# Performance work log

Measured on AMD Instinct MI355X. Metric: run time of the kernel, lower is better.

The kernel has to match this reference:

```python
import jax, jax.numpy as jnp
import numpy as np

B, N, D_IN, D_MEM, LAYERS = 8, 2048, 128, 128, 3


def setup_inputs() -> dict:
    key = jax.random.key(0)
    k1, k2, k3, k4 = jax.random.split(key, 4)
    inputs = jax.random.normal(k1, (B, N, D_IN), dtype=jnp.float32)
    # attention-derived adjacency: nonnegative weights
    out_adj = jax.random.uniform(k2, (B, N, N), dtype=jnp.float32)
    # per-layer Linear weights (all layers 128->128 here, stacked) with
    # torch nn.Linear-style init scale 1/sqrt(fan_in)
    scale = 1.0 / np.sqrt(D_IN)
    W = jax.random.uniform(k3, (LAYERS, D_IN, D_MEM), minval=-scale, maxval=scale, dtype=jnp.float32)
    b = jax.random.uniform(k4, (LAYERS, D_MEM), minval=-scale, maxval=scale, dtype=jnp.float32)
    return {"inputs": inputs, "out_adj": out_adj, "W": W, "b": b}


def reference(inputs, out_adj, W, b):
    # GCN.forward (eval mode; dropout = identity)
    adj = out_adj  # [B, N, N]
    denom = jnp.sum(adj, axis=2, keepdims=True) + 1.0  # [B, N, 1]
    outputs = inputs  # [B, N, D]
    for l in range(W.shape[0]):
        Ax = jnp.einsum('bij,bjd->bid', adj, outputs)      # aggregate
        AxW = Ax @ W[l] + b[l]                             # per-layer linear
        outputs = jax.nn.relu(AxW / denom)                 # normalize + activate
    return outputs
```

## Files before the change

### kernel.cpp

```cpp
#include <hip/hip_runtime.h>

#define NN 2048
#define DD 128

typedef _Float16 f16x8 __attribute__((ext_vector_type(8)));
typedef float f32x4 __attribute__((ext_vector_type(4)));

__global__ __launch_bounds__(256) void prep_kernel(
    const float* __restrict__ W, _Float16* __restrict__ Wt) {
  int idx = blockIdx.x * 256 + threadIdx.x;
  int l = idx >> 14, r = idx & 16383, d = r >> 7, k = r & 127;
  Wt[idx] = (_Float16)W[l * 16384 + k * 128 + d];
}

__global__ __launch_bounds__(256) void gemmY_kernel(
    const float* __restrict__ X, const _Float16* __restrict__ Wt,
    _Float16* __restrict__ Yt) {
  const int bx = blockIdx.x;
  const int batch = bx & 7, n0 = (bx >> 3) * 32;
  const int tid = threadIdx.x, lane = tid & 63, wave = tid >> 6;
  const int quad = lane >> 4, l15 = lane & 15, d0 = wave * 32;
  const float* Xb = X + (size_t)(batch * NN + n0) * DD;
  f32x4 acc[2][2] = {};
#pragma unroll
  for (int kk = 0; kk < 128; kk += 32) {
    f16x8 a0 = *(const f16x8*)(Wt + (d0 + l15) * DD + kk + quad * 8);
    f16x8 a1 = *(const f16x8*)(Wt + (d0 + 16 + l15) * DD + kk + quad * 8);
#pragma unroll
    for (int fi = 0; fi < 2; ++fi) {
      const float* xp = Xb + (size_t)(fi * 16 + l15) * DD + kk + quad * 8;
      float4 x0 = *(const float4*)xp;
      float4 x1 = *(const float4*)(xp + 4);
      f16x8 b = {(_Float16)x0.x, (_Float16)x0.y, (_Float16)x0.z, (_Float16)x0.w,
                 (_Float16)x1.x, (_Float16)x1.y, (_Float16)x1.z, (_Float16)x1.w};
      acc[0][fi] = __builtin_amdgcn_mfma_f32_16x16x32_f16(a0, b, acc[0][fi], 0, 0, 0);
      acc[1][fi] = __builtin_amdgcn_mfma_f32_16x16x32_f16(a1, b, acc[1][fi], 0, 0, 0);
    }
  }
  _Float16* YtB = Yt + (size_t)batch * DD * NN;
#pragma unroll
  for (int df = 0; df < 2; ++df)
#pragma unroll
    for (int fi = 0; fi < 2; ++fi)
#pragma unroll
      for (int r = 0; r < 4; ++r)
        YtB[(size_t)(d0 + df * 16 + quad * 4 + r) * NN + n0 + fi * 16 + l15] =
            (_Float16)acc[df][fi][r];
}

template<bool LAST>
__global__ __launch_bounds__(256) void agg_kernel(
    const float* __restrict__ adj, const _Float16* __restrict__ Yt,
    const float* __restrict__ bias, const _Float16* __restrict__ Wn,
    _Float16* __restrict__ Ytn, float* __restrict__ out) {
  __shared__ _Float16 Bs[2][32 * 64];
  __shared__ float Xs[32][132];
  __shared__ float bsh[128];
  __shared__ float rd[32];

  const int tid = threadIdx.x, bx = blockIdx.x;
  const int batch = bx & 7, i0 = (bx >> 3) * 32;
  const int lane = tid & 63, wave = tid >> 6;
  const int quad = lane >> 4, l15 = lane & 15, d0 = wave * 32;
  const int ai = tid >> 3, ac = tid & 7;
  const int sc = ac ^ (ai & 7);

  const float* adjR = adj + (size_t)(batch * NN + i0 + ai) * NN + ac * 8;
  const _Float16* YtB = Yt + (size_t)batch * DD * NN;
  const _Float16* Ya0 = YtB + (size_t)(d0 + l15) * NN;
  const _Float16* Ya1 = YtB + (size_t)(d0 + 16 + l15) * NN;

  if (tid < 128) bsh[tid] = bias[tid];

  f32x4 acc[2][2] = {};
  float rowsum = 0.f;

  float4 av0 = *(const float4*)(adjR);
  float4 av1 = *(const float4*)(adjR + 4);
  f16x8 a[2][2];
#pragma unroll
  for (int k2 = 0; k2 < 2; ++k2) {
    a[k2][0] = *(const f16x8*)(Ya0 + k2 * 32 + quad * 8);
    a[k2][1] = *(const f16x8*)(Ya1 + k2 * 32 + quad * 8);
  }

  for (int ko = 0; ko < 32; ++ko) {
    rowsum += ((av0.x + av0.y) + (av0.z + av0.w)) + ((av1.x + av1.y) + (av1.z + av1.w));
    f16x8 h = {(_Float16)av0.x, (_Float16)av0.y, (_Float16)av0.z, (_Float16)av0.w,
               (_Float16)av1.x, (_Float16)av1.y, (_Float16)av1.z, (_Float16)av1.w};
    *(f16x8*)(&Bs[ko & 1][ai * 64 + sc * 8]) = h;
    f16x8 an[2][2];
    if (ko < 31) {
      const int kb = (ko + 1) * 64;
      av0 = *(const float4*)(adjR + kb);
      av1 = *(const float4*)(adjR + kb + 4);
#pragma unroll
      for (int k2 = 0; k2 < 2; ++k2) {
        an[k2][0] = *(const f16x8*)(Ya0 + kb + k2 * 32 + quad * 8);
        an[k2][1] = *(const f16x8*)(Ya1 + kb + k2 * 32 + quad * 8);
      }
    }
    __syncthreads();
    const _Float16* B = Bs[ko & 1];
#pragma unroll
    for (int k2 = 0; k2 < 2; ++k2)
#pragma unroll
      for (int fi = 0; fi < 2; ++fi) {
        const int row = fi * 16 + l15;
        const int ch = (k2 * 4 + quad) ^ (row & 7);
        f16x8 b = *(const f16x8*)(&B[row * 64 + ch * 8]);
        acc[0][fi] = __builtin_amdgcn_mfma_f32_16x16x32_f16(a[k2][0], b, acc[0][fi], 0, 0, 0);
        acc[1][fi] = __builtin_amdgcn_mfma_f32_16x16x32_f16(a[k2][1], b, acc[1][fi], 0, 0, 0);
      }
#pragma unroll
    for (int k2 = 0; k2 < 2; ++k2) { a[k2][0] = an[k2][0]; a[k2][1] = an[k2][1]; }
  }

  rowsum += __shfl_xor(rowsum, 1);
  rowsum += __shfl_xor(rowsum, 2);
  rowsum += __shfl_xor(rowsum, 4);
  if (ac == 0) rd[ai] = 1.0f / (rowsum + 1.0f);
  __syncthreads();

#pragma unroll
  for (int df = 0; df < 2; ++df)
#pragma unroll
    for (int fi = 0; fi < 2; ++fi)
#pragma unroll
      for (int r = 0; r < 4; ++r) {
        int d = d0 + df * 16 + quad * 4 + r;
        int i = fi * 16 + l15;
        Xs[i][d] = fmaxf((acc[df][fi][r] + bsh[d]) * rd[i], 0.f);
      }
  __syncthreads();

  if (LAST) {
    float* outB = out + (size_t)(batch * NN + i0) * DD;
#pragma unroll
    for (int u = 0; u < 4; ++u) {
      int c = tid + 256 * u;
      int i = c >> 5, f4 = (c & 31) * 4;
      *(float4*)(outB + (size_t)i * DD + f4) = *(const float4*)&Xs[i][f4];
    }
  } else {
    f32x4 acc2[2][2] = {};
#pragma unroll
    for (int kk = 0; kk < 128; kk += 32) {
      f16x8 a0 = *(const f16x8*)(Wn + (d0 + l15) * DD + kk + quad * 8);
      f16x8 a1 = *(const f16x8*)(Wn + (d0 + 16 + l15) * DD + kk + quad * 8);
#pragma unroll
      for (int fi = 0; fi < 2; ++fi) {
        const float* xp = &Xs[fi * 16 + l15][kk + quad * 8];
        f16x8 b = {(_Float16)xp[0], (_Float16)xp[1], (_Float16)xp[2], (_Float16)xp[3],
                   (_Float16)xp[4], (_Float16)xp[5], (_Float16)xp[6], (_Float16)xp[7]};
        acc2[0][fi] = __builtin_amdgcn_mfma_f32_16x16x32_f16(a0, b, acc2[0][fi], 0, 0, 0);
        acc2[1][fi] = __builtin_amdgcn_mfma_f32_16x16x32_f16(a1, b, acc2[1][fi], 0, 0, 0);
      }
    }
    _Float16* YnB = Ytn + (size_t)batch * DD * NN;
#pragma unroll
    for (int df = 0; df < 2; ++df)
#pragma unroll
      for (int fi = 0; fi < 2; ++fi)
#pragma unroll
        for (int r = 0; r < 4; ++r)
          YnB[(size_t)(d0 + df * 16 + quad * 4 + r) * NN + i0 + fi * 16 + l15] =
              (_Float16)acc2[df][fi][r];
  }
}

extern "C" void kernel_launch(void* const* d_in, const int* in_sizes, int n_in,
                              void* d_out, int out_size, void* d_ws, size_t ws_size,
                              hipStream_t stream) {
  const float* x0   = (const float*)d_in[0];
  const float* adj  = (const float*)d_in[1];
  const float* W    = (const float*)d_in[2];
  const float* bias = (const float*)d_in[3];
  float* out = (float*)d_out;

  _Float16* Wt   = (_Float16*)d_ws;
  _Float16* YtA  = (_Float16*)((char*)d_ws + 131072);
  _Float16* YtB_ = (_Float16*)d_out;

  dim3 blk(256);
  prep_kernel <<<192, blk, 0, stream>>>(W, Wt);
  gemmY_kernel<<<512, blk, 0, stream>>>(x0, Wt, YtA);
  agg_kernel<false><<<512, blk, 0, stream>>>(adj, YtA,  bias,       Wt + 16384, YtB_, nullptr);
  agg_kernel<false><<<512, blk, 0, stream>>>(adj, YtB_, bias + 128, Wt + 32768, YtA,  nullptr);
  agg_kernel<true ><<<512, blk, 0, stream>>>(adj, YtA,  bias + 256, nullptr,    nullptr, out);
}
```

Measured before the change: 290.0 us.

## Cache fp16 adjacency and row normalizers on first layer, reuse in later layers

The first aggregation layer writes the fp16-converted adjacency tile and the per-row reciprocal normalizers to workspace. A new fp16 aggregation kernel then reads that half-size adjacency directly into MFMA fragments, with no LDS staging or barriers, for layers two and three. This halves adjacency read traffic for those layers at the cost of an extra 64 MB write in layer one. It needs a large workspace and falls back to the old path when the workspace is too small.

```diff
diff --git a/kernel.cpp b/kernel.cpp
--- a/kernel.cpp
+++ b/kernel.cpp
@@ -48,11 +48,12 @@
             (_Float16)acc[df][fi][r];
 }
 
-template<bool LAST>
+template<bool SAVE, bool LAST>
 __global__ __launch_bounds__(256) void agg_kernel(
     const float* __restrict__ adj, const _Float16* __restrict__ Yt,
     const float* __restrict__ bias, const _Float16* __restrict__ Wn,
-    _Float16* __restrict__ Ytn, float* __restrict__ out) {
+    _Float16* __restrict__ Ytn, float* __restrict__ out,
+    _Float16* __restrict__ adjH, float* __restrict__ rdg) {
   __shared__ _Float16 Bs[2][32 * 64];
   __shared__ float Xs[32][132];
   __shared__ float bsh[128];
@@ -69,6 +70,7 @@
   const _Float16* YtB = Yt + (size_t)batch * DD * NN;
   const _Float16* Ya0 = YtB + (size_t)(d0 + l15) * NN;
   const _Float16* Ya1 = YtB + (size_t)(d0 + 16 + l15) * NN;
+  _Float16* AdjHW = SAVE ? adjH + (size_t)(batch * NN + i0 + ai) * NN + ac * 8 : nullptr;
 
   if (tid < 128) bsh[tid] = bias[tid];
 
@@ -89,6 +91,7 @@
     f16x8 h = {(_Float16)av0.x, (_Float16)av0.y, (_Float16)av0.z, (_Float16)av0.w,
                (_Float16)av1.x, (_Float16)av1.y, (_Float16)av1.z, (_Float16)av1.w};
     *(f16x8*)(&Bs[ko & 1][ai * 64 + sc * 8]) = h;
+    if (SAVE) *(f16x8*)(AdjHW + ko * 64) = h;
     f16x8 an[2][2];
     if (ko < 31) {
       const int kb = (ko + 1) * 64;
@@ -119,7 +122,11 @@
   rowsum += __shfl_xor(rowsum, 1);
   rowsum += __shfl_xor(rowsum, 2);
   rowsum += __shfl_xor(rowsum, 4);
-  if (ac == 0) rd[ai] = 1.0f / (rowsum + 1.0f);
+  if (ac == 0) {
+    float v = 1.0f / (rowsum + 1.0f);
+    rd[ai] = v;
+    if (SAVE) rdg[batch * NN + i0 + ai] = v;
+  }
   __syncthreads();
 
 #pragma unroll
@@ -131,6 +138,114 @@
         int d = d0 + df * 16 + quad * 4 + r;
         int i = fi * 16 + l15;
         Xs[i][d] = fmaxf((acc[df][fi][r] + bsh[d]) * rd[i], 0.f);
+      }
+  __syncthreads();
+
+  if (LAST) {
+    float* outB = out + (size_t)(batch * NN + i0) * DD;
+#pragma unroll
+    for (int u = 0; u < 4; ++u) {
+      int c = tid + 256 * u;
+      int i = c >> 5, f4 = (c & 31) * 4;
+      *(float4*)(outB + (size_t)i * DD + f4) = *(const float4*)&Xs[i][f4];
+    }
+  } else {
+    f32x4 acc2[2][2] = {};
+#pragma unroll
+    for (int kk = 0; kk < 128; kk += 32) {
+      f16x8 a0 = *(const f16x8*)(Wn + (d0 + l15) * DD + kk + quad * 8);
+      f16x8 a1 = *(const f16x8*)(Wn + (d0 + 16 + l15) * DD + kk + quad * 8);
+#pragma unroll
+      for (int fi = 0; fi < 2; ++fi) {
+        const float* xp = &Xs[fi * 16 + l15][kk + quad * 8];
+        f16x8 b = {(_Float16)xp[0], (_Float16)xp[1], (_Float16)xp[2], (_Float16)xp[3],
+                   (_Float16)xp[4], (_Float16)xp[5], (_Float16)xp[6], (_Float16)xp[7]};
+        acc2[0][fi] = __builtin_amdgcn_mfma_f32_16x16x32_f16(a0, b, acc2[0][fi], 0, 0, 0);
+        acc2[1][fi] = __builtin_amdgcn_mfma_f32_16x16x32_f16(a1, b, acc2[1][fi], 0, 0, 0);
+      }
+    }
+    _Float16* YnB = Ytn + (size_t)batch * DD * NN;
+#pragma unroll
+    for (int df = 0; df < 2; ++df)
+#pragma unroll
+      for (int fi = 0; fi < 2; ++fi)
+#pragma unroll
+        for (int r = 0; r < 4; ++r)
+          YnB[(size_t)(d0 + df * 16 + quad * 4 + r) * NN + i0 + fi * 16 + l15] =
+              (_Float16)acc2[df][fi][r];
+  }
+}
+
+__device__ __forceinline__ void loadf16(f16x8 (&AF)[2][2], f16x8 (&BF)[2][2],
+    const _Float16* Ya0, const _Float16* Ya1,
+    const _Float16* Ba0, const _Float16* Ba1, int kb) {
+#pragma unroll
+  for (int k2 = 0; k2 < 2; ++k2) {
+    AF[k2][0] = *(const f16x8*)(Ya0 + kb + k2 * 32);
+    AF[k2][1] = *(const f16x8*)(Ya1 + kb + k2 * 32);
+    BF[k2][0] = *(const f16x8*)(Ba0 + kb + k2 * 32);
+    BF[k2][1] = *(const f16x8*)(Ba1 + kb + k2 * 32);
+  }
+}
+
+__device__ __forceinline__ void mfma8(const f16x8 (&AF)[2][2],
+    const f16x8 (&BF)[2][2], f32x4 (&acc)[2][2]) {
+#pragma unroll
+  for (int k2 = 0; k2 < 2; ++k2)
+#pragma unroll
+    for (int fi = 0; fi < 2; ++fi) {
+      acc[0][fi] = __builtin_amdgcn_mfma_f32_16x16x32_f16(AF[k2][0], BF[k2][fi], acc[0][fi], 0, 0, 0);
+      acc[1][fi] = __builtin_amdgcn_mfma_f32_16x16x32_f16(AF[k2][1], BF[k2][fi], acc[1][fi], 0, 0, 0);
+    }
+}
+
+template<bool LAST>
+__global__ __launch_bounds__(256) void aggf16_kernel(
+    const _Float16* __restrict__ adjH, const float* __restrict__ rdg,
+    const _Float16* __restrict__ Yt, const float* __restrict__ bias,
+    const _Float16* __restrict__ Wn, _Float16* __restrict__ Ytn,
+    float* __restrict__ out) {
+  __shared__ float Xs[32][132];
+
+  const int tid = threadIdx.x, bx = blockIdx.x;
+  const int batch = bx & 7, i0 = (bx >> 3) * 32;
+  const int lane = tid & 63, wave = tid >> 6;
+  const int quad = lane >> 4, l15 = lane & 15, d0 = wave * 32;
+
+  const _Float16* YtB = Yt + (size_t)batch * DD * NN;
+  const _Float16* Ya0 = YtB + (size_t)(d0 + l15) * NN + quad * 8;
+  const _Float16* Ya1 = YtB + (size_t)(d0 + 16 + l15) * NN + quad * 8;
+  const _Float16* AdjB = adjH + (size_t)(batch * NN + i0) * NN;
+  const _Float16* Ba0 = AdjB + (size_t)l15 * NN + quad * 8;
+  const _Float16* Ba1 = AdjB + (size_t)(16 + l15) * NN + quad * 8;
+
+  const float* rdb = rdg + batch * NN + i0;
+  float rdv0 = rdb[l15], rdv1 = rdb[16 + l15];
+  float4 bv0 = *(const float4*)(bias + d0 + quad * 4);
+  float4 bv1 = *(const float4*)(bias + d0 + 16 + quad * 4);
+
+  f32x4 acc[2][2] = {};
+  f16x8 aA[2][2], bA[2][2], aB[2][2], bB[2][2];
+
+  loadf16(aA, bA, Ya0, Ya1, Ba0, Ba1, 0);
+#pragma unroll
+  for (int ko = 0; ko < 32; ko += 2) {
+    if (ko + 1 < 32) loadf16(aB, bB, Ya0, Ya1, Ba0, Ba1, (ko + 1) * 64);
+    mfma8(aA, bA, acc);
+    if (ko + 2 < 32) loadf16(aA, bA, Ya0, Ya1, Ba0, Ba1, (ko + 2) * 64);
+    mfma8(aB, bB, acc);
+  }
+
+#pragma unroll
+  for (int df = 0; df < 2; ++df)
+#pragma unroll
+    for (int fi = 0; fi < 2; ++fi)
+#pragma unroll
+      for (int r = 0; r < 4; ++r) {
+        int d = d0 + df * 16 + quad * 4 + r;
+        float bia = df ? ((const float*)&bv1)[r] : ((const float*)&bv0)[r];
+        float rv = fi ? rdv1 : rdv0;
+        Xs[fi * 16 + l15][d] = fmaxf((acc[df][fi][r] + bia) * rv, 0.f);
       }
   __syncthreads();
 
@@ -180,12 +295,22 @@
 
   _Float16* Wt   = (_Float16*)d_ws;
   _Float16* YtA  = (_Float16*)((char*)d_ws + 131072);
+  float*    rdg  = (float*)((char*)d_ws + 131072 + (4u << 20));
+  _Float16* adjH = (_Float16*)((char*)d_ws + (8u << 20));
   _Float16* YtB_ = (_Float16*)d_out;
+
+  const bool big = ws_size >= ((8ull + 64ull) << 20);
 
   dim3 blk(256);
   prep_kernel <<<192, blk, 0, stream>>>(W, Wt);
   gemmY_kernel<<<512, blk, 0, stream>>>(x0, Wt, YtA);
-  agg_kernel<false><<<512, blk, 0, stream>>>(adj, YtA,  bias,       Wt + 16384, YtB_, nullptr);
-  agg_kernel<false><<<512, blk, 0, stream>>>(adj, YtB_, bias + 128, Wt + 32768, YtA,  nullptr);
-  agg_kernel<true ><<<512, blk, 0, stream>>>(adj, YtA,  bias + 256, nullptr,    nullptr, out);
-}
+  if (big) {
+    agg_kernel<true, false><<<512, blk, 0, stream>>>(adj, YtA, bias, Wt + 16384, YtB_, nullptr, adjH, rdg);
+    aggf16_kernel<false><<<512, blk, 0, stream>>>(adjH, rdg, YtB_, bias + 128, Wt + 32768, YtA, nullptr);
+    aggf16_kernel<true ><<<512, blk, 0, stream>>>(adjH, rdg, YtA, bias + 256, nullptr, nullptr, out);
+  } else {
+    agg_kernel<false, false><<<512, blk, 0, stream>>>(adj, YtA,  bias,       Wt + 16384, YtB_, nullptr, nullptr, nullptr);
+    agg_kernel<false, false><<<512, blk, 0, stream>>>(adj, YtB_, bias + 128, Wt + 32768, YtA,  nullptr, nullptr, nullptr);
+    agg_kernel<false, true ><<<512, blk, 0, stream>>>(adj, YtA,  bias + 256, nullptr,    nullptr, out, nullptr, nullptr);
+  }
+}
```

New measurement: 350.3 us. +20.8%, slower.

## Pre-convert adjacency to fp16 fragment-tiled layout and fuse row sums

Applied to the files above, without the earlier changes.

Adds a pass that reads the fp32 adjacency once, stores it as fp16 in an MFMA-fragment-tiled layout, and computes the normalisation reciprocals. Each of the three aggregation kernels then streams half the bytes and needs no LDS staging or synchronisation in its main loop. Inputs and intermediates are likewise kept in a pre-tiled layout, and the first layer reorders to aggregate before the linear. This needs a large workspace (gated on its size) and adds a full extra write and read of the fp16 adjacency.

```diff
diff --git a/kernel.cpp b/kernel.cpp
--- a/kernel.cpp
+++ b/kernel.cpp
@@ -5,12 +5,218 @@
 
 typedef _Float16 f16x8 __attribute__((ext_vector_type(8)));
 typedef float f32x4 __attribute__((ext_vector_type(4)));
+
 
 __global__ __launch_bounds__(256) void prep_kernel(
     const float* __restrict__ W, _Float16* __restrict__ Wt) {
   int idx = blockIdx.x * 256 + threadIdx.x;
   int l = idx >> 14, r = idx & 16383, d = r >> 7, k = r & 127;
   Wt[idx] = (_Float16)W[l * 16384 + k * 128 + d];
+}
+
+__global__ __launch_bounds__(256) void prepAdj_kernel(
+    const float* __restrict__ adj, _Float16* __restrict__ adjH,
+    float* __restrict__ rdg) {
+  __shared__ float rs[16][4];
+  const int bx = blockIdx.x, tid = threadIdx.x;
+  const int it = bx & 127, batch = bx >> 7;
+  const int lane = tid & 63, wave = tid >> 6;
+  const int quad = lane >> 4, l15 = lane & 15;
+
+  const float* Ap = adj + ((size_t)(batch * NN) + it * 16 + l15) * NN + quad * 8;
+  _Float16* Hp = adjH + (size_t)batch * NN * NN + ((size_t)it * 64) * 512 + lane * 8;
+
+  float s = 0.f;
+#pragma unroll
+  for (int j = 0; j < 16; ++j) {
+    const int ct = wave + 4 * j;
+    float4 a0 = *(const float4*)(Ap + ct * 32);
+    float4 a1 = *(const float4*)(Ap + ct * 32 + 4);
+    s += ((a0.x + a0.y) + (a0.z + a0.w)) + ((a1.x + a1.y) + (a1.z + a1.w));
+    f16x8 h = {(_Float16)a0.x, (_Float16)a0.y, (_Float16)a0.z, (_Float16)a0.w,
+               (_Float16)a1.x, (_Float16)a1.y, (_Float16)a1.z, (_Float16)a1.w};
+    *(f16x8*)(Hp + (size_t)ct * 512) = h;
+  }
+  s += __shfl_xor(s, 16);
+  s += __shfl_xor(s, 32);
+  if (lane < 16) rs[lane][wave] = s;
+  __syncthreads();
+  if (tid < 16) {
+    float t = rs[tid][0] + rs[tid][1] + rs[tid][2] + rs[tid][3];
+    rdg[batch * NN + it * 16 + tid] = 1.0f / (t + 1.0f);
+  }
+}
+
+__global__ __launch_bounds__(256) void transposeX_kernel(
+    const float* __restrict__ X, _Float16* __restrict__ Xt) {
+  const int bx = blockIdx.x, tid = threadIdx.x;
+  const int batch = bx & 7, nt = bx >> 3;
+  const int lane = tid & 63, wave = tid >> 6;
+  const int quad = lane >> 4, l15 = lane & 15;
+  const size_t batA = (size_t)batch * (128 * NN);
+#pragma unroll
+  for (int dtl = 0; dtl < 2; ++dtl) {
+    const int dt = wave * 2 + dtl;
+    const float* Xp = X + ((size_t)(batch * NN) + nt * 32 + quad * 8) * DD + dt * 16 + l15;
+    f16x8 v;
+#pragma unroll
+    for (int e = 0; e < 8; ++e) v[e] = (_Float16)Xp[(size_t)e * DD];
+    *(f16x8*)(Xt + batA + ((size_t)(dt * 64 + nt)) * 512 + lane * 8) = v;
+  }
+}
+
+__device__ __forceinline__ void epiGemm(const float (*Xs)[132],
+    const _Float16* __restrict__ Wf, int d0, int quad, int l15,
+    f32x4 (&o)[2][2]) {
+#pragma unroll
+  for (int kk = 0; kk < 128; kk += 32) {
+    f16x8 a0 = *(const f16x8*)(Wf + (d0 + l15) * DD + kk + quad * 8);
+    f16x8 a1 = *(const f16x8*)(Wf + (d0 + 16 + l15) * DD + kk + quad * 8);
+#pragma unroll
+    for (int fi = 0; fi < 2; ++fi) {
+      const float* xp = &Xs[fi * 16 + l15][kk + quad * 8];
+      f16x8 b = {(_Float16)xp[0], (_Float16)xp[1], (_Float16)xp[2], (_Float16)xp[3],
+                 (_Float16)xp[4], (_Float16)xp[5], (_Float16)xp[6], (_Float16)xp[7]};
+      o[0][fi] = __builtin_amdgcn_mfma_f32_16x16x32_f16(a0, b, o[0][fi], 0, 0, 0);
+      o[1][fi] = __builtin_amdgcn_mfma_f32_16x16x32_f16(a1, b, o[1][fi], 0, 0, 0);
+    }
+  }
+}
+
+template<int MODE>
+__global__ __launch_bounds__(256, 4) void aggT_kernel(
+    const _Float16* __restrict__ adjH, const float* __restrict__ rdg,
+    const _Float16* __restrict__ At, const float* __restrict__ bias,
+    const _Float16* __restrict__ WA, const _Float16* __restrict__ WB,
+    _Float16* __restrict__ Yout, float* __restrict__ out) {
+  __shared__ float Xs[32][132];
+  __shared__ float bsh[128];
+  __shared__ float rdsh[32];
+
+  const int tid = threadIdx.x, bx = blockIdx.x;
+  const int batch = bx & 7, i0 = (bx >> 3) * 32;
+  const int lane = tid & 63, wave = tid >> 6;
+  const int quad = lane >> 4, l15 = lane & 15, d0 = wave * 32;
+
+  const size_t batA = (size_t)batch * (128 * NN);
+  const size_t batB = (size_t)batch * ((size_t)NN * NN);
+  const int it0 = i0 >> 4;
+  const _Float16* Ap0 = At + batA + ((size_t)(2 * wave) * 64) * 512 + lane * 8;
+  const _Float16* Ap1 = At + batA + ((size_t)(2 * wave + 1) * 64) * 512 + lane * 8;
+  const _Float16* Bp0 = adjH + batB + ((size_t)it0 * 64) * 512 + lane * 8;
+  const _Float16* Bp1 = adjH + batB + ((size_t)(it0 + 1) * 64) * 512 + lane * 8;
+
+  if (tid < 128) bsh[tid] = bias[tid];
+  if (tid < 32) rdsh[tid] = rdg[batch * NN + i0 + tid];
+  __syncthreads();
+
+  f32x4 acc[2][2] = {};
+  f16x8 qa0[2], qa1[2], qb0[2], qb1[2];
+#define LDT(ct, s)                                  \
+  { qa0[s] = *(const f16x8*)(Ap0 + (ct) * 512);     \
+    qa1[s] = *(const f16x8*)(Ap1 + (ct) * 512);     \
+    qb0[s] = *(const f16x8*)(Bp0 + (ct) * 512);     \
+    qb1[s] = *(const f16x8*)(Bp1 + (ct) * 512); }
+#define MMT(s)                                                                          \
+  { acc[0][0] = __builtin_amdgcn_mfma_f32_16x16x32_f16(qa0[s], qb0[s], acc[0][0], 0, 0, 0); \
+    acc[0][1] = __builtin_amdgcn_mfma_f32_16x16x32_f16(qa0[s], qb1[s], acc[0][1], 0, 0, 0); \
+    acc[1][0] = __builtin_amdgcn_mfma_f32_16x16x32_f16(qa1[s], qb0[s], acc[1][0], 0, 0, 0); \
+    acc[1][1] = __builtin_amdgcn_mfma_f32_16x16x32_f16(qa1[s], qb1[s], acc[1][1], 0, 0, 0); }
+
+  LDT(0, 0)
+  LDT(1, 1)
+#pragma unroll
+  for (int ct = 0; ct < 64; ct += 2) {
+    MMT(0)
+    if (ct + 2 < 64) LDT(ct + 2, 0)
+    MMT(1)
+    if (ct + 3 < 64) LDT(ct + 3, 1)
+  }
+#undef LDT
+#undef MMT
+
+  const float rv0 = rdsh[l15], rv1 = rdsh[16 + l15];
+
+  f32x4 accY[2][2];
+
+  if (MODE == 0) {
+#pragma unroll
+    for (int df = 0; df < 2; ++df)
+#pragma unroll
+      for (int fi = 0; fi < 2; ++fi)
+#pragma unroll
+        for (int r = 0; r < 4; ++r)
+          Xs[fi * 16 + l15][d0 + df * 16 + quad * 4 + r] = acc[df][fi][r];
+    __syncthreads();
+    f32x4 acc2[2][2] = {};
+    epiGemm(Xs, WA, d0, quad, l15, acc2);
+    __syncthreads();
+#pragma unroll
+    for (int df = 0; df < 2; ++df)
+#pragma unroll
+      for (int fi = 0; fi < 2; ++fi)
+#pragma unroll
+        for (int r = 0; r < 4; ++r) {
+          int d = d0 + df * 16 + quad * 4 + r;
+          float rv = fi ? rv1 : rv0;
+          Xs[fi * 16 + l15][d] = fmaxf((acc2[df][fi][r] + bsh[d]) * rv, 0.f);
+        }
+    __syncthreads();
+    f32x4 acc3[2][2] = {};
+    epiGemm(Xs, WB, d0, quad, l15, acc3);
+#pragma unroll
+    for (int df = 0; df < 2; ++df)
+#pragma unroll
+      for (int fi = 0; fi < 2; ++fi) accY[df][fi] = acc3[df][fi];
+  } else {
+#pragma unroll
+    for (int df = 0; df < 2; ++df)
+#pragma unroll
+      for (int fi = 0; fi < 2; ++fi)
+#pragma unroll
+        for (int r = 0; r < 4; ++r) {
+          int d = d0 + df * 16 + quad * 4 + r;
+          float rv = fi ? rv1 : rv0;
+          Xs[fi * 16 + l15][d] = fmaxf((acc[df][fi][r] + bsh[d]) * rv, 0.f);
+        }
+    __syncthreads();
+    if (MODE == 2) {
+      float* outB = out + (size_t)(batch * NN + i0) * DD;
+#pragma unroll
+      for (int u = 0; u < 4; ++u) {
+        int c = tid + 256 * u;
+        int i = c >> 5, f4 = (c & 31) * 4;
+        *(float4*)(outB + (size_t)i * DD + f4) = *(const float4*)&Xs[i][f4];
+      }
+      return;
+    }
+    f32x4 acc2[2][2] = {};
+    epiGemm(Xs, WA, d0, quad, l15, acc2);
+#pragma unroll
+    for (int df = 0; df < 2; ++df)
+#pragma unroll
+      for (int fi = 0; fi < 2; ++fi) accY[df][fi] = acc2[df][fi];
+  }
+
+  __syncthreads();
+  _Float16* Yst = (_Float16*)Xs;
+#pragma unroll
+  for (int df = 0; df < 2; ++df)
+#pragma unroll
+    for (int fi = 0; fi < 2; ++fi)
+#pragma unroll
+      for (int r = 0; r < 4; ++r)
+        Yst[(d0 + df * 16 + quad * 4 + r) * 40 + fi * 16 + l15] =
+            (_Float16)accY[df][fi][r];
+  __syncthreads();
+  const int nt = i0 >> 5;
+  _Float16* Yb = Yout + batA;
+#pragma unroll
+  for (int dtl = 0; dtl < 2; ++dtl) {
+    const int dt = 2 * wave + dtl;
+    f16x8 v = *(const f16x8*)(&Yst[(dt * 16 + l15) * 40 + quad * 8]);
+    *(f16x8*)(Yb + ((size_t)(dt * 64 + nt)) * 512 + lane * 8) = v;
+  }
 }
 
 __global__ __launch_bounds__(256) void gemmY_kernel(
@@ -144,19 +350,7 @@
     }
   } else {
     f32x4 acc2[2][2] = {};
-#pragma unroll
-    for (int kk = 0; kk < 128; kk += 32) {
-      f16x8 a0 = *(const f16x8*)(Wn + (d0 + l15) * DD + kk + quad * 8);
-      f16x8 a1 = *(const f16x8*)(Wn + (d0 + 16 + l15) * DD + kk + quad * 8);
-#pragma unroll
-      for (int fi = 0; fi < 2; ++fi) {
-        const float* xp = &Xs[fi * 16 + l15][kk + quad * 8];
-        f16x8 b = {(_Float16)xp[0], (_Float16)xp[1], (_Float16)xp[2], (_Float16)xp[3],
-                   (_Float16)xp[4], (_Float16)xp[5], (_Float16)xp[6], (_Float16)xp[7]};
-        acc2[0][fi] = __builtin_amdgcn_mfma_f32_16x16x32_f16(a0, b, acc2[0][fi], 0, 0, 0);
-        acc2[1][fi] = __builtin_amdgcn_mfma_f32_16x16x32_f16(a1, b, acc2[1][fi], 0, 0, 0);
-      }
-    }
+    epiGemm(Xs, Wn, d0, quad, l15, acc2);
     _Float16* YnB = Ytn + (size_t)batch * DD * NN;
 #pragma unroll
     for (int df = 0; df < 2; ++df)
@@ -179,13 +373,28 @@
   float* out = (float*)d_out;
 
   _Float16* Wt   = (_Float16*)d_ws;
-  _Float16* YtA  = (_Float16*)((char*)d_ws + 131072);
-  _Float16* YtB_ = (_Float16*)d_out;
+  float*    rdg  = (float*)((char*)d_ws + (1u << 17));
+  _Float16* Xt   = (_Float16*)((char*)d_ws + (1u << 20));
+  _Float16* Y1t  = (_Float16*)((char*)d_ws + (5u << 20));
+  _Float16* Y2t  = (_Float16*)((char*)d_ws + (9u << 20));
+  _Float16* adjH = (_Float16*)((char*)d_ws + (16u << 20));
+
+  const bool big = ws_size >= (80ull << 20);
 
   dim3 blk(256);
-  prep_kernel <<<192, blk, 0, stream>>>(W, Wt);
-  gemmY_kernel<<<512, blk, 0, stream>>>(x0, Wt, YtA);
-  agg_kernel<false><<<512, blk, 0, stream>>>(adj, YtA,  bias,       Wt + 16384, YtB_, nullptr);
-  agg_kernel<false><<<512, blk, 0, stream>>>(adj, YtB_, bias + 128, Wt + 32768, YtA,  nullptr);
-  agg_kernel<true ><<<512, blk, 0, stream>>>(adj, YtA,  bias + 256, nullptr,    nullptr, out);
-}
+  prep_kernel<<<192, blk, 0, stream>>>(W, Wt);
+  if (big) {
+    prepAdj_kernel  <<<1024, blk, 0, stream>>>(adj, adjH, rdg);
+    transposeX_kernel<<<512, blk, 0, stream>>>(x0, Xt);
+    aggT_kernel<0><<<512, blk, 0, stream>>>(adjH, rdg, Xt, bias, Wt, Wt + 16384, Y1t, nullptr);
+    aggT_kernel<1><<<512, blk, 0, stream>>>(adjH, rdg, Y1t, bias + 128, Wt + 32768, nullptr, Y2t, nullptr);
+    aggT_kernel<2><<<512, blk, 0, stream>>>(adjH, rdg, Y2t, bias + 256, nullptr, nullptr, nullptr, out);
+  } else {
+    _Float16* YtA  = Xt;
+    _Float16* YtB_ = (_Float16*)d_out;
+    gemmY_kernel<<<512, blk, 0, stream>>>(x0, Wt, YtA);
+    agg_kernel<false><<<512, blk, 0, stream>>>(adj, YtA,  bias,       Wt + 16384, YtB_, nullptr);
+    agg_kernel<false><<<512, blk, 0, stream>>>(adj, YtB_, bias + 128, Wt + 32768, YtA,  nullptr);
+    agg_kernel<true ><<<512, blk, 0, stream>>>(adj, YtA,  bias + 256, nullptr,    nullptr, out);
+  }
+}
```

Measured after the change: 294.4 us. About the same (+1.5%).
